# Kernel optimization log

Hardware: AMD Instinct MI355X
Metric: run time of the kernel (lower is better)

Reference implementation:

```python
import jax, jax.numpy as jnp
import numpy as np

B, S, D, H = 2, 2048, 1024, 16
HD = D // H

def setup_inputs() -> dict:
    key = jax.random.key(0)
    ks = jax.random.split(key, 7)
    s = 1.0 / np.sqrt(D)
    return {
        "x": jax.random.normal(ks[0], (B, S, D), dtype=jnp.float32),
        "Wq": jax.random.uniform(ks[1], (D, D), jnp.float32, -s, s),
        "bq": jax.random.uniform(ks[2], (D,), jnp.float32, -s, s),
        "Wk": jax.random.uniform(ks[3], (D, D), jnp.float32, -s, s),
        "bk": jax.random.uniform(ks[4], (D,), jnp.float32, -s, s),
        "Wv": jax.random.uniform(ks[5], (D, D), jnp.float32, -s, s),
        "bv": jax.random.uniform(ks[6], (D,), jnp.float32, -s, s),
    }

def reference(x, Wq, bq, Wk, bk, Wv, bv):
    b, s, d = x.shape
    def proj(W, bias):
        # [b,s,d] -> [b,H,s,hd]
        y = x @ W + bias
        return y.reshape(b, s, H, HD).transpose(0, 2, 1, 3)
    Q = proj(Wq, bq)
    K = proj(Wk, bk)
    V = proj(Wv, bv)
    # NOTE: original scales by head_dim**0.5 (not sqrt) -> divide by sqrt(HD)
    scores = jnp.einsum("bhqd,bhkd->bhqk", Q, K) / (HD ** 0.5)
    attn = jax.nn.softmax(scores, axis=-1)
    out = jnp.einsum("bhqk,bhkd->bhqd", attn, V)
    out = out.transpose(0, 2, 1, 3).reshape(b, s, d)
    return out + x
```

## Files before the change

### kernel.cpp

```cpp
#include <hip/hip_runtime.h>
#include <stdint.h>

typedef float f32x4 __attribute__((ext_vector_type(4)));
typedef __bf16 bf16x8 __attribute__((ext_vector_type(8)));

union Frag {
    bf16x8 v;
    uint32_t u[4];
    __bf16 e[8];
    uint4 q;
};

constexpr int B_ = 2, S_ = 2048, D_ = 1024, H_ = 16, HD_ = 64;
constexpr int M_ = B_ * S_;

__host__ __device__ constexpr int kperm(int kl) {
    return ((kl & 12) << 1) | ((kl & 16) >> 2) | (kl & 3);
}

typedef const __attribute__((address_space(1))) char gch_t;
typedef __attribute__((address_space(3))) char lch_t;
#define GLD(g, l) __builtin_amdgcn_global_load_lds((gch_t*)(g), (lch_t*)(l), 16, 0, 0)

#define MFMA16(a, b, c) __builtin_amdgcn_mfma_f32_16x16x32_bf16((a), (b), (c), 0, 0, 0)

__global__ void k_cast_x(const float* __restrict__ x, __bf16* __restrict__ xb) {
    int t = blockIdx.x * 256 + threadIdx.x;
    const float4* src = (const float4*)(x + (size_t)t * 32);
    __bf16 buf[32];
#pragma unroll
    for (int j = 0; j < 8; ++j) {
        float4 f = src[j];
        buf[kperm(4 * j + 0)] = (__bf16)f.x;
        buf[kperm(4 * j + 1)] = (__bf16)f.y;
        buf[kperm(4 * j + 2)] = (__bf16)f.z;
        buf[kperm(4 * j + 3)] = (__bf16)f.w;
    }
    uint4* dst = (uint4*)(xb + (size_t)t * 32);
#pragma unroll
    for (int j = 0; j < 4; ++j) dst[j] = ((const uint4*)buf)[j];
}

__global__ void k_prep_w(const float* __restrict__ Wq, const float* __restrict__ Wk,
                         const float* __restrict__ Wv, __bf16* __restrict__ Wt) {
    __shared__ float tile[32][33];
    int p = blockIdx.z;
    const float* W = (p == 0) ? Wq : (p == 1 ? Wk : Wv);
    int n0 = blockIdx.x * 32, k0 = blockIdx.y * 32;
    int tx = threadIdx.x, ty = threadIdx.y;
#pragma unroll
    for (int t = 0; t < 4; ++t)
        tile[ty + 8 * t][tx] = W[(size_t)(k0 + ty + 8 * t) * D_ + n0 + tx];
    __syncthreads();
#pragma unroll
    for (int t = 0; t < 4; ++t)
        Wt[(size_t)(p * D_ + n0 + ty + 8 * t) * D_ + k0 + kperm(tx)] = (__bf16)tile[tx][ty + 8 * t];
}

__global__ __launch_bounds__(256) void k_qkv(
        const __bf16* __restrict__ xb, const __bf16* __restrict__ Wt,
        const float* __restrict__ bq, const float* __restrict__ bk, const float* __restrict__ bv,
        __bf16* __restrict__ Qb, __bf16* __restrict__ Kb, __bf16* __restrict__ Vt) {
    __shared__ __align__(16) char ldsA[2][128 * 128];
    __shared__ __align__(16) char ldsB[2][128 * 128];

    const int tid = threadIdx.x;
    const int m0 = blockIdx.x * 128, n0 = blockIdx.y * 128;
    const int lane = tid & 63, w = tid >> 6;
    const int wr = w >> 1, wc = w & 1;
    const int g = lane >> 4, qr = lane & 15, qr7 = qr & 7;
    const int lr = lane >> 3, lp = lane & 7;
    const int c = lp ^ lr;

    const __bf16* aSrc = xb + (size_t)(m0 + w * 32 + lr) * D_ + c * 8;
    const __bf16* bSrc = Wt + (size_t)(n0 + w * 32 + lr) * D_ + c * 8;
    const int dstOff = (w * 32) * 128;

    f32x4 acc[4][4] = {};

    auto STAGE = [&](int buf, int kk) {
#pragma unroll
        for (int j = 0; j < 4; ++j) {
            GLD(aSrc + kk + j * (8 * D_), ldsA[buf] + dstOff + j * (8 * 128));
            GLD(bSrc + kk + j * (8 * D_), ldsB[buf] + dstOff + j * (8 * 128));
        }
    };
    auto COMPUTE = [&](int buf) {
#pragma unroll
        for (int kc = 0; kc < 2; ++kc) {
            Frag afr[4], bfr[4];
#pragma unroll
            for (int mi = 0; mi < 4; ++mi) {
                int r = wr * 64 + mi * 16 + qr;
                afr[mi].q = *(const uint4*)(ldsA[buf] + r * 128 + (((4 * kc + g) ^ qr7) << 4));
            }
#pragma unroll
            for (int ni = 0; ni < 4; ++ni) {
                int r = wc * 64 + ni * 16 + qr;
                bfr[ni].q = *(const uint4*)(ldsB[buf] + r * 128 + (((4 * kc + g) ^ qr7) << 4));
            }
#pragma unroll
            for (int mi = 0; mi < 4; ++mi)
#pragma unroll
                for (int ni = 0; ni < 4; ++ni)
                    acc[mi][ni] = MFMA16(afr[mi].v, bfr[ni].v, acc[mi][ni]);
        }
    };

    STAGE(0, 0);
    __syncthreads();
    for (int t = 0; t < 14; t += 2) {
        STAGE(1, (t + 1) * 64);
        COMPUTE(0);
        __syncthreads();
        STAGE(0, (t + 2) * 64);
        COMPUTE(1);
        __syncthreads();
    }
    STAGE(1, 15 * 64);
    COMPUTE(0);
    __syncthreads();
    COMPUTE(1);

    const int p = n0 >> 10;
    const float* bias = (p == 0) ? bq : (p == 1 ? bk : bv);
#pragma unroll
    for (int ni = 0; ni < 4; ++ni) {
        int n = n0 + wc * 64 + ni * 16 + qr;
        int d = n & 1023;
        float bb = bias[d];
        int h = d >> 6, hd = d & 63;
        int hd_s = (hd & 32) | kperm(hd & 31);
#pragma unroll
        for (int mi = 0; mi < 4; ++mi) {
#pragma unroll
            for (int r = 0; r < 4; ++r) {
                int m = m0 + wr * 64 + mi * 16 + 4 * g + r;
                float vv = acc[mi][ni][r] + bb;
                int b = m >> 11, s = m & 2047;
                if (p == 0) {
                    vv *= 0.125f;
                    Qb[((size_t)((b * H_ + h) * S_ + s)) * HD_ + hd_s] = (__bf16)vv;
                } else if (p == 1) {
                    Kb[((size_t)((b * H_ + h) * S_ + s)) * HD_ + hd_s] = (__bf16)vv;
                } else {
                    int s_s = (s & ~31) | kperm(s & 31);
                    Vt[((size_t)((b * H_ + h) * HD_ + hd)) * S_ + s_s] = (__bf16)vv;
                }
            }
        }
    }
}

__global__ __launch_bounds__(256) void k_attn(
        const __bf16* __restrict__ Qb, const __bf16* __restrict__ Kb,
        const __bf16* __restrict__ Vt, const float* __restrict__ x,
        float* __restrict__ out) {
    __shared__ __align__(16) char ldsK[2][64 * 128];
    __shared__ __align__(16) char ldsV[2][64 * 128];

    const int tid = threadIdx.x;
    const int q0 = blockIdx.x * 64;
    const int bh = blockIdx.y;
    const int lane = tid & 63, w = tid >> 6;
    const int g = lane >> 4, qr = lane & 15, qr7 = qr & 7;
    const int lr = lane >> 3, lp = lane & 7;
    const int c = lp ^ lr;
    const int qrow = q0 + w * 16 + qr;

    Frag qf[2];
    const __bf16* qp = Qb + ((size_t)bh * S_ + qrow) * HD_;
    qf[0].q = *(const uint4*)(qp + g * 8);
    qf[1].q = *(const uint4*)(qp + 32 + g * 8);

    const __bf16* kSrc = Kb + ((size_t)bh * S_ + w * 16 + lr) * HD_ + c * 8;
    const __bf16* vSrc = Vt + ((size_t)bh * HD_ + w * 16 + lr) * S_ + c * 8;
    const int dstOff = (w * 16) * 128;

    f32x4 oacc[4] = {};
    f32x4 lacc = {};
    float mrun = -INFINITY;
    const float L2E = 1.44269504f;
    const float THR = 5.545177f;

    Frag ones;
    ones.u[0] = ones.u[1] = ones.u[2] = ones.u[3] = 0x3f803f80u;

    auto STAGE = [&](int buf, int kv0) {
        GLD(kSrc + (size_t)kv0 * HD_,           ldsK[buf] + dstOff);
        GLD(kSrc + (size_t)kv0 * HD_ + 8 * HD_, ldsK[buf] + dstOff + 8 * 128);
        GLD(vSrc + kv0,                         ldsV[buf] + dstOff);
        GLD(vSrc + kv0 + 8 * S_,                ldsV[buf] + dstOff + 8 * 128);
    };

    auto TILE = [&](int buf) {
        f32x4 sc[4];
        __builtin_amdgcn_s_setprio(1);
#pragma unroll
        for (int kt = 0; kt < 4; ++kt) {
            const char* base = ldsK[buf] + (kt * 16 + qr) * 128;
            Frag k0, k1;
            k0.q = *(const uint4*)(base + ((g ^ qr7) << 4));
            k1.q = *(const uint4*)(base + (((4 + g) ^ qr7) << 4));
            f32x4 z = {};
            z = MFMA16(k0.v, qf[0].v, z);
            z = MFMA16(k1.v, qf[1].v, z);
            sc[kt] = z;
        }
        __builtin_amdgcn_s_setprio(0);

        float tmax = -INFINITY;
#pragma unroll
        for (int kt = 0; kt < 4; ++kt)
#pragma unroll
            for (int r = 0; r < 4; ++r) tmax = fmaxf(tmax, sc[kt][r]);
        tmax = fmaxf(tmax, __shfl_xor(tmax, 16, 64));
        tmax = fmaxf(tmax, __shfl_xor(tmax, 32, 64));

        if (__any(tmax > mrun + THR)) {
            float mnew = fmaxf(mrun, tmax);
            float scale = __builtin_amdgcn_exp2f((mrun - mnew) * L2E);
            mrun = mnew;
            float scr[4];
#pragma unroll
            for (int r = 0; r < 4; ++r) scr[r] = __shfl(scale, (lane & 48) | (4 * g + r), 64);
#pragma unroll
            for (int ni = 0; ni < 4; ++ni)
#pragma unroll
                for (int r = 0; r < 4; ++r) oacc[ni][r] *= scr[r];
#pragma unroll
            for (int r = 0; r < 4; ++r) lacc[r] *= scr[r];
        }

        float m2 = mrun * L2E;
        Frag pa[2];
#pragma unroll
        for (int r = 0; r < 4; ++r) {
            pa[0].e[r]     = (__bf16)__builtin_amdgcn_exp2f(fmaf(sc[0][r], L2E, -m2));
            pa[0].e[4 + r] = (__bf16)__builtin_amdgcn_exp2f(fmaf(sc[1][r], L2E, -m2));
            pa[1].e[r]     = (__bf16)__builtin_amdgcn_exp2f(fmaf(sc[2][r], L2E, -m2));
            pa[1].e[4 + r] = (__bf16)__builtin_amdgcn_exp2f(fmaf(sc[3][r], L2E, -m2));
        }

        __builtin_amdgcn_s_setprio(1);
        lacc = MFMA16(pa[0].v, ones.v, lacc);
        lacc = MFMA16(pa[1].v, ones.v, lacc);

#pragma unroll
        for (int ni = 0; ni < 4; ++ni) {
            const char* base = ldsV[buf] + (ni * 16 + qr) * 128;
            Frag v0, v1;
            v0.q = *(const uint4*)(base + ((g ^ qr7) << 4));
            v1.q = *(const uint4*)(base + (((4 + g) ^ qr7) << 4));
            oacc[ni] = MFMA16(pa[0].v, v0.v, oacc[ni]);
            oacc[ni] = MFMA16(pa[1].v, v1.v, oacc[ni]);
        }
        __builtin_amdgcn_s_setprio(0);
    };

    STAGE(0, 0);
    __syncthreads();
    for (int t = 0; t < 30; t += 2) {
        STAGE(1, (t + 1) * 64);
        TILE(0);
        __syncthreads();
        STAGE(0, (t + 2) * 64);
        TILE(1);
        __syncthreads();
    }
    STAGE(1, 31 * 64);
    TILE(0);
    __syncthreads();
    TILE(1);

    float rs[4];
#pragma unroll
    for (int r = 0; r < 4; ++r) rs[r] = 1.0f / lacc[r];

    int b = bh >> 4, h = bh & 15;
#pragma unroll
    for (int ni = 0; ni < 4; ++ni) {
#pragma unroll
        for (int r = 0; r < 4; ++r) {
            int q = q0 + w * 16 + 4 * g + r;
            size_t addr = ((size_t)(b * S_ + q)) * D_ + h * 64 + ni * 16 + qr;
            out[addr] = oacc[ni][r] * rs[r] + x[addr];
        }
    }
}

extern "C" void kernel_launch(void* const* d_in, const int* in_sizes, int n_in,
                              void* d_out, int out_size, void* d_ws, size_t ws_size,
                              hipStream_t stream) {
    const float* x  = (const float*)d_in[0];
    const float* Wq = (const float*)d_in[1];
    const float* bq = (const float*)d_in[2];
    const float* Wk = (const float*)d_in[3];
    const float* bk = (const float*)d_in[4];
    const float* Wv = (const float*)d_in[5];
    const float* bv = (const float*)d_in[6];
    float* out = (float*)d_out;

    char* ws = (char*)d_ws;
    __bf16* xb = (__bf16*)(ws);
    __bf16* Wt = (__bf16*)(ws + 8388608);
    __bf16* Qb = (__bf16*)(ws + 14680064);
    __bf16* Kb = (__bf16*)(ws + 23068672);
    __bf16* Vt = (__bf16*)(ws + 31457280);

    k_cast_x<<<512, 256, 0, stream>>>(x, xb);
    k_prep_w<<<dim3(32, 32, 3), dim3(32, 8), 0, stream>>>(Wq, Wk, Wv, Wt);
    k_qkv<<<dim3(32, 24), 256, 0, stream>>>(xb, Wt, bq, bk, bv, Qb, Kb, Vt);
    k_attn<<<dim3(32, 32), 256, 0, stream>>>(Qb, Kb, Vt, x, out);
}
```

Before: 118.0 us.

## Rewrite QKV GEMM with 256x256 tiles, 8 waves, interleaved prefetch and XCD-aware mapping

The QKV projection GEMM moves from 128x128 tiles with 4 waves to 256x256 tiles with 8 waves and 128KB of LDS. Global-to-LDS loads for future k-steps are interleaved between MFMA quarter-steps, using explicit vmcnt/lgkmcnt waits, barriers and setprio. A 1D grid remaps block IDs so that blocks on the same XCD share A and B panels for L2 reuse. The goal is higher arithmetic intensity and better overlap of loads with MFMA, at the cost of fewer blocks (192) and much more register and LDS pressure.

Result: slower. 127.8 us (+8.4%).

```diff
diff --git a/kernel.cpp b/kernel.cpp
--- a/kernel.cpp
+++ b/kernel.cpp
@@ -57,85 +57,123 @@
         Wt[(size_t)(p * D_ + n0 + ty + 8 * t) * D_ + k0 + kperm(tx)] = (__bf16)tile[tx][ty + 8 * t];
 }
 
-__global__ __launch_bounds__(256) void k_qkv(
+__global__ __launch_bounds__(512, 2) void k_qkv(
         const __bf16* __restrict__ xb, const __bf16* __restrict__ Wt,
         const float* __restrict__ bq, const float* __restrict__ bk, const float* __restrict__ bv,
         __bf16* __restrict__ Qb, __bf16* __restrict__ Kb, __bf16* __restrict__ Vt) {
-    __shared__ __align__(16) char ldsA[2][128 * 128];
-    __shared__ __align__(16) char ldsB[2][128 * 128];
+    __shared__ __align__(16) char lds[131072];
 
     const int tid = threadIdx.x;
-    const int m0 = blockIdx.x * 128, n0 = blockIdx.y * 128;
-    const int lane = tid & 63, w = tid >> 6;
-    const int wr = w >> 1, wc = w & 1;
+    const int lane = tid & 63, wid = tid >> 6;
+    const int wr = wid >> 2, wc = wid & 3;
     const int g = lane >> 4, qr = lane & 15, qr7 = qr & 7;
     const int lr = lane >> 3, lp = lane & 7;
     const int c = lp ^ lr;
-
-    const __bf16* aSrc = xb + (size_t)(m0 + w * 32 + lr) * D_ + c * 8;
-    const __bf16* bSrc = Wt + (size_t)(n0 + w * 32 + lr) * D_ + c * 8;
-    const int dstOff = (w * 32) * 128;
-
-    f32x4 acc[4][4] = {};
-
-    auto STAGE = [&](int buf, int kk) {
-#pragma unroll
-        for (int j = 0; j < 4; ++j) {
-            GLD(aSrc + kk + j * (8 * D_), ldsA[buf] + dstOff + j * (8 * 128));
-            GLD(bSrc + kk + j * (8 * D_), ldsB[buf] + dstOff + j * (8 * 128));
-        }
-    };
-    auto COMPUTE = [&](int buf) {
-#pragma unroll
-        for (int kc = 0; kc < 2; ++kc) {
-            Frag afr[4], bfr[4];
-#pragma unroll
-            for (int mi = 0; mi < 4; ++mi) {
-                int r = wr * 64 + mi * 16 + qr;
-                afr[mi].q = *(const uint4*)(ldsA[buf] + r * 128 + (((4 * kc + g) ^ qr7) << 4));
-            }
-#pragma unroll
-            for (int ni = 0; ni < 4; ++ni) {
-                int r = wc * 64 + ni * 16 + qr;
-                bfr[ni].q = *(const uint4*)(ldsB[buf] + r * 128 + (((4 * kc + g) ^ qr7) << 4));
-            }
-#pragma unroll
-            for (int mi = 0; mi < 4; ++mi)
-#pragma unroll
-                for (int ni = 0; ni < 4; ++ni)
-                    acc[mi][ni] = MFMA16(afr[mi].v, bfr[ni].v, acc[mi][ni]);
-        }
-    };
-
-    STAGE(0, 0);
-    __syncthreads();
+    const int wofs = wid * 1024;
+
+    int bid = blockIdx.x;
+    int xcd = bid & 7, local = bid >> 3;
+    int mx = ((xcd & 3) << 2) | (local & 3);
+    int ny = (xcd >> 2) * 6 + (local >> 2);
+    const int m0 = mx * 256, n0 = ny * 256;
+
+    const __bf16* aBase = xb + (size_t)(m0 + wid * 8 + lr) * D_ + c * 8;
+    const __bf16* bBase = Wt + (size_t)(n0 + wid * 8 + lr) * D_ + c * 8;
+
+#define GA(s_, kt_, qa_) GLD(aBase + (size_t)((qa_) * 64) * D_ + (kt_) * 64, \
+                             lds + (s_) * 32768 + (qa_) * 8192 + wofs)
+#define GB(s_, kt_, gb_) GLD(bBase + (size_t)((gb_) * 64) * D_ + (kt_) * 64, \
+                             lds + 65536 + (s_) * 32768 + (gb_) * 8192 + wofs)
+
+    f32x4 acc[8][4] = {};
+    Frag bfr[4][2];
+    Frag afr[2][2];
+
+#define BARR() __builtin_amdgcn_s_barrier()
+#define LGKM0() do { asm volatile("s_waitcnt lgkmcnt(0)" ::: "memory"); \
+                     __builtin_amdgcn_sched_barrier(0); } while (0)
+
+#define LDA(As_, q_) do { \
+    _Pragma("unroll") \
+    for (int j = 0; j < 2; ++j) \
+    _Pragma("unroll") \
+        for (int kc = 0; kc < 2; ++kc) \
+            afr[j][kc].q = *(const uint4*)((As_) + ((2 * (q_) + j) * 32 + wr * 16 + qr) * 128 + \
+                                           (((4 * kc + g) ^ qr7) << 4)); \
+} while (0)
+
+#define LDB(Bs_) do { \
+    _Pragma("unroll") \
+    for (int ni = 0; ni < 4; ++ni) \
+    _Pragma("unroll") \
+        for (int kc = 0; kc < 2; ++kc) \
+            bfr[ni][kc].q = *(const uint4*)((Bs_) + ((ni) * 64 + wc * 16 + qr) * 128 + \
+                                            (((4 * kc + g) ^ qr7) << 4)); \
+} while (0)
+
+#define MMQ(q_) do { \
+    __builtin_amdgcn_s_setprio(1); \
+    _Pragma("unroll") \
+    for (int j = 0; j < 2; ++j) \
+    _Pragma("unroll") \
+        for (int ni = 0; ni < 4; ++ni) \
+    _Pragma("unroll") \
+            for (int kc = 0; kc < 2; ++kc) \
+                acc[2 * (q_) + j][ni] = MFMA16(afr[j][kc].v, bfr[ni][kc].v, acc[2 * (q_) + j][ni]); \
+    __builtin_amdgcn_s_setprio(0); \
+} while (0)
+
+#define TILE(s_, kt_, NSTR) do { \
+    char* As = lds + (s_) * 32768; \
+    char* Bs = lds + 65536 + (s_) * 32768; \
+    asm volatile("s_waitcnt vmcnt(" NSTR ")" ::: "memory"); \
+    BARR(); \
+     \
+    LDB(Bs); LDA(As, 0); \
+    if ((kt_) < 15) GA(1 - (s_), (kt_) + 1, 3); \
+    BARR(); LGKM0(); MMQ(0); BARR(); \
+     \
+    LDA(As, 1); \
+    if ((kt_) < 14) { GA((s_), (kt_) + 2, 0); GB((s_), (kt_) + 2, 0); GB((s_), (kt_) + 2, 1); } \
+    BARR(); LGKM0(); MMQ(1); BARR(); \
+     \
+    LDA(As, 2); \
+    if ((kt_) < 14) { GA((s_), (kt_) + 2, 1); GB((s_), (kt_) + 2, 2); GB((s_), (kt_) + 2, 3); } \
+    BARR(); LGKM0(); MMQ(2); BARR(); \
+     \
+    LDA(As, 3); \
+    if ((kt_) < 14) GA((s_), (kt_) + 2, 2); \
+    BARR(); LGKM0(); MMQ(3); \
+} while (0)
+
+    GA(0, 0, 0); GA(0, 0, 1); GA(0, 0, 2);
+    GB(0, 0, 0); GB(0, 0, 1); GB(0, 0, 2); GB(0, 0, 3);
+    GA(0, 0, 3);
+    GA(1, 1, 0); GB(1, 1, 0); GB(1, 1, 1);
+    GA(1, 1, 1); GB(1, 1, 2); GB(1, 1, 3);
+    GA(1, 1, 2);
+
     for (int t = 0; t < 14; t += 2) {
-        STAGE(1, (t + 1) * 64);
-        COMPUTE(0);
-        __syncthreads();
-        STAGE(0, (t + 2) * 64);
-        COMPUTE(1);
-        __syncthreads();
-    }
-    STAGE(1, 15 * 64);
-    COMPUTE(0);
-    __syncthreads();
-    COMPUTE(1);
+        TILE(0, t, "7");
+        TILE(1, t + 1, "7");
+    }
+    TILE(0, 14, "7");
+    TILE(1, 15, "0");
 
     const int p = n0 >> 10;
     const float* bias = (p == 0) ? bq : (p == 1 ? bk : bv);
 #pragma unroll
     for (int ni = 0; ni < 4; ++ni) {
-        int n = n0 + wc * 64 + ni * 16 + qr;
+        int n = n0 + ni * 64 + wc * 16 + qr;
         int d = n & 1023;
         float bb = bias[d];
         int h = d >> 6, hd = d & 63;
         int hd_s = (hd & 32) | kperm(hd & 31);
 #pragma unroll
-        for (int mi = 0; mi < 4; ++mi) {
+        for (int mi = 0; mi < 8; ++mi) {
 #pragma unroll
             for (int r = 0; r < 4; ++r) {
-                int m = m0 + wr * 64 + mi * 16 + 4 * g + r;
+                int m = m0 + mi * 32 + wr * 16 + 4 * g + r;
                 float vv = acc[mi][ni][r] + bb;
                 int b = m >> 11, s = m & 2047;
                 if (p == 0) {
@@ -150,6 +188,14 @@
             }
         }
     }
+#undef GA
+#undef GB
+#undef BARR
+#undef LGKM0
+#undef LDA
+#undef LDB
+#undef MMQ
+#undef TILE
 }
 
 __global__ __launch_bounds__(256) void k_attn(
@@ -310,6 +356,6 @@
 
     k_cast_x<<<512, 256, 0, stream>>>(x, xb);
     k_prep_w<<<dim3(32, 32, 3), dim3(32, 8), 0, stream>>>(Wq, Wk, Wv, Wt);
-    k_qkv<<<dim3(32, 24), 256, 0, stream>>>(xb, Wt, bq, bk, bv, Qb, Kb, Vt);
+    k_qkv<<<192, 512, 0, stream>>>(xb, Wt, bq, bk, bv, Qb, Kb, Vt);
     k_attn<<<dim3(32, 32), 256, 0, stream>>>(Qb, Kb, Vt, x, out);
 }
```

## Use 8 waves per QKV GEMM tile and swizzle block order

Applied to the files above, without the earlier changes.

The QKV projection GEMM now runs 512 threads (8 waves in a 2x4 grid) per 128x128 tile instead of 4 waves, so each wave holds a 64x32 sub-tile with half the accumulators and issues half the async global-to-LDS loads. The launch becomes a flat 1D grid with a block-index swizzle that groups consecutive blocks by column tile to improve L2 reuse of the weight and activation tiles. This aims to raise latency hiding through more resident waves and lower register pressure, at the cost of more redundant LDS fragment reads for A across the column waves.

Measured after the change: 126.6 us. +7.3%, slower.

```diff
diff --git a/kernel.cpp b/kernel.cpp
--- a/kernel.cpp
+++ b/kernel.cpp
@@ -57,52 +57,54 @@
         Wt[(size_t)(p * D_ + n0 + ty + 8 * t) * D_ + k0 + kperm(tx)] = (__bf16)tile[tx][ty + 8 * t];
 }
 
-__global__ __launch_bounds__(256) void k_qkv(
+__global__ __launch_bounds__(512, 4) void k_qkv(
         const __bf16* __restrict__ xb, const __bf16* __restrict__ Wt,
         const float* __restrict__ bq, const float* __restrict__ bk, const float* __restrict__ bv,
         __bf16* __restrict__ Qb, __bf16* __restrict__ Kb, __bf16* __restrict__ Vt) {
-    __shared__ __align__(16) char ldsA[2][128 * 128];
-    __shared__ __align__(16) char ldsB[2][128 * 128];
+    __shared__ __align__(16) char ldsA[2][16384];
+    __shared__ __align__(16) char ldsB[2][16384];
 
     const int tid = threadIdx.x;
-    const int m0 = blockIdx.x * 128, n0 = blockIdx.y * 128;
-    const int lane = tid & 63, w = tid >> 6;
-    const int wr = w >> 1, wc = w & 1;
+    const int lane = tid & 63, wid = tid >> 6;
+    const int wr = wid >> 2, wc = wid & 3;
     const int g = lane >> 4, qr = lane & 15, qr7 = qr & 7;
     const int lr = lane >> 3, lp = lane & 7;
     const int c = lp ^ lr;
 
-    const __bf16* aSrc = xb + (size_t)(m0 + w * 32 + lr) * D_ + c * 8;
-    const __bf16* bSrc = Wt + (size_t)(n0 + w * 32 + lr) * D_ + c * 8;
-    const int dstOff = (w * 32) * 128;
-
-    f32x4 acc[4][4] = {};
+    int bid = blockIdx.x;
+    int swz = (bid & 7) * 96 + (bid >> 3);
+    const int m0 = (swz & 31) * 128, n0 = (swz >> 5) * 128;
+
+    const __bf16* aSrc = xb + (size_t)(m0 + wid * 16 + lr) * D_ + c * 8;
+    const __bf16* bSrc = Wt + (size_t)(n0 + wid * 16 + lr) * D_ + c * 8;
+    const int dstOff = wid * 16 * 128;
+
+    f32x4 acc[4][2] = {};
 
     auto STAGE = [&](int buf, int kk) {
-#pragma unroll
-        for (int j = 0; j < 4; ++j) {
-            GLD(aSrc + kk + j * (8 * D_), ldsA[buf] + dstOff + j * (8 * 128));
-            GLD(bSrc + kk + j * (8 * D_), ldsB[buf] + dstOff + j * (8 * 128));
-        }
+        GLD(aSrc + kk,          ldsA[buf] + dstOff);
+        GLD(aSrc + kk + 8 * D_, ldsA[buf] + dstOff + 8 * 128);
+        GLD(bSrc + kk,          ldsB[buf] + dstOff);
+        GLD(bSrc + kk + 8 * D_, ldsB[buf] + dstOff + 8 * 128);
     };
     auto COMPUTE = [&](int buf) {
 #pragma unroll
         for (int kc = 0; kc < 2; ++kc) {
-            Frag afr[4], bfr[4];
+            Frag afr[4], bfr[2];
 #pragma unroll
             for (int mi = 0; mi < 4; ++mi) {
                 int r = wr * 64 + mi * 16 + qr;
                 afr[mi].q = *(const uint4*)(ldsA[buf] + r * 128 + (((4 * kc + g) ^ qr7) << 4));
             }
 #pragma unroll
-            for (int ni = 0; ni < 4; ++ni) {
-                int r = wc * 64 + ni * 16 + qr;
+            for (int ni = 0; ni < 2; ++ni) {
+                int r = wc * 32 + ni * 16 + qr;
                 bfr[ni].q = *(const uint4*)(ldsB[buf] + r * 128 + (((4 * kc + g) ^ qr7) << 4));
             }
 #pragma unroll
             for (int mi = 0; mi < 4; ++mi)
 #pragma unroll
-                for (int ni = 0; ni < 4; ++ni)
+                for (int ni = 0; ni < 2; ++ni)
                     acc[mi][ni] = MFMA16(afr[mi].v, bfr[ni].v, acc[mi][ni]);
         }
     };
@@ -125,8 +127,8 @@
     const int p = n0 >> 10;
     const float* bias = (p == 0) ? bq : (p == 1 ? bk : bv);
 #pragma unroll
-    for (int ni = 0; ni < 4; ++ni) {
-        int n = n0 + wc * 64 + ni * 16 + qr;
+    for (int ni = 0; ni < 2; ++ni) {
+        int n = n0 + wc * 32 + ni * 16 + qr;
         int d = n & 1023;
         float bb = bias[d];
         int h = d >> 6, hd = d & 63;
@@ -310,6 +312,6 @@
 
     k_cast_x<<<512, 256, 0, stream>>>(x, xb);
     k_prep_w<<<dim3(32, 32, 3), dim3(32, 8), 0, stream>>>(Wq, Wk, Wv, Wt);
-    k_qkv<<<dim3(32, 24), 256, 0, stream>>>(xb, Wt, bq, bk, bv, Qb, Kb, Vt);
+    k_qkv<<<768, 512, 0, stream>>>(xb, Wt, bq, bk, bv, Qb, Kb, Vt);
     k_attn<<<dim3(32, 32), 256, 0, stream>>>(Qb, Kb, Vt, x, out);
 }
```
